# Kernel tuning notes

Hardware: AMD Instinct MI355X
Metric: run time of the kernel (lower is better)

The kernel has to match this reference:

```python
import jax, jax.numpy as jnp
import numpy as np

WINDOW = 8
NUM_HEADS = 12


def setup_inputs() -> dict:
    key = jax.random.key(0)
    k1, k2, k3 = jax.random.split(key, 3)
    B, H, W, C = 32, 64, 64, 384
    x = jax.random.normal(k1, (B, H, W, C), dtype=jnp.float32)
    w_qkv = jax.random.normal(k2, (C, 3 * C), dtype=jnp.float32) * (C ** -0.5)
    w_proj = jax.random.normal(k3, (C, C), dtype=jnp.float32) * (C ** -0.5)
    b_proj = jnp.zeros((C,), dtype=jnp.float32)
    return {"x": x, "w_qkv": w_qkv, "w_proj": w_proj, "b_proj": b_proj}


def window_partition(x, ws):
    B, H, W, C = x.shape
    x = x.reshape(B, H // ws, ws, W // ws, ws, C)
    x = x.transpose(0, 1, 3, 2, 4, 5)  # [B, nH, nW, ws, ws, C]
    return x.reshape(-1, ws * ws, C)


def window_reverse(x, ws, H, W):
    nWin = (H // ws) * (W // ws)
    B = x.shape[0] // nWin
    C = x.shape[2]
    x = x.reshape(B, H // ws, W // ws, ws, ws, C)
    x = x.transpose(0, 1, 3, 2, 4, 5)
    return x.reshape(B, H, W, C)


def reference(x, w_qkv, w_proj, b_proj):
    B, H, W, C = x.shape
    ws = WINDOW
    nh = NUM_HEADS
    hd = C // nh
    scale = hd ** -0.5
    N = ws * ws

    xw = window_partition(x, ws)                      # [nW*B, N, C]
    qkv = xw @ w_qkv                                  # [nW*B, N, 3C]
    qkv = qkv.reshape(-1, N, 3, nh, hd)
    qkv = qkv.transpose(2, 0, 3, 1, 4)                # [3, nW*B, nh, N, hd]
    q, k, v = qkv[0], qkv[1], qkv[2]

    attn = jnp.einsum('whnd,whmd->whnm', q, k) * scale  # [nW*B, nh, N, N]
    attn = jax.nn.softmax(attn, axis=-1)
    out = jnp.einsum('whnm,whmd->whnd', attn, v)         # [nW*B, nh, N, hd]
    out = out.transpose(0, 2, 1, 3).reshape(-1, N, C)    # [nW*B, N, C]
    out = out @ w_proj + b_proj
    return window_reverse(out, ws, H, W)
```

## Files before the change

kernel.cpp:

```cpp
#include <hip/hip_runtime.h>


typedef __attribute__((ext_vector_type(8))) short bf16x8;
typedef __attribute__((ext_vector_type(4))) float f32x4;
typedef __attribute__((ext_vector_type(4))) short short4_t;

__device__ __forceinline__ short f2bf(float f) {
    union { float f; unsigned u; } v; v.f = f;
    unsigned r = v.u + 0x7fffu + ((v.u >> 16) & 1u);
    return (short)(r >> 16);
}

__device__ __forceinline__ unsigned pk2(float a, float b) {
    return ((unsigned)(unsigned short)f2bf(b) << 16) | (unsigned short)f2bf(a);
}

__device__ __forceinline__ f32x4 mfma16(bf16x8 a, bf16x8 b, f32x4 c) {
    return __builtin_amdgcn_mfma_f32_16x16x32_bf16(a, b, c, 0, 0, 0);
}

__device__ __forceinline__ short4_t pack4(f32x4 v) {
    short4_t s;
    s.x = f2bf(v[0]); s.y = f2bf(v[1]); s.z = f2bf(v[2]); s.w = f2bf(v[3]);
    return s;
}

__device__ __forceinline__ void gload_lds16(const void* g, void* l) {
    __builtin_amdgcn_global_load_lds(
        (const __attribute__((address_space(1))) unsigned int*)g,
        (__attribute__((address_space(3))) unsigned int*)l, 16, 0, 0);
}

__global__ void prep_weights(const float* __restrict__ wqkv, const float* __restrict__ wproj,
                             short* __restrict__ wq_sw, short* __restrict__ wp_t) {
    const int QKV_ELEMS = 12 * 96 * 384;
    int i = blockIdx.x * 256 + threadIdx.x;
    if (i < QKV_ELEMS) {
        int h = i / (96 * 384);
        int o = i % (96 * 384);
        int row = o / 384;
        int kb = ((o % 384) * 2) ^ ((row & 7) << 4);
        int k = kb >> 1;
        int col = (row >> 5) * 384 + h * 32 + (row & 31);
        float w = wqkv[k * 1152 + col];
        if (row < 32) w *= 0.17677669529663687f;
        wq_sw[i] = f2bf(w);
    } else if (i < QKV_ELEMS + 384 * 384) {
        int j = i - QKV_ELEMS;
        int n = j / 384, k = j % 384;
        wp_t[j] = f2bf(wproj[k * 384 + n]);
    }
}

__global__ __launch_bounds__(1024)
void qkv_attn(const float* __restrict__ x, const short* __restrict__ wq_sw,
              short* __restrict__ y_sw) {
    __shared__ short Wl[96 * 384];
    __shared__ short k_s[4][64 * 40];
    __shared__ short v_t[4][32 * 72];
    __shared__ short ps[4][64 * 72];

    const int tid   = threadIdx.x;
    const int lane  = tid & 63;
    const int wv    = tid >> 6;
    const int col16 = lane & 15;
    const int kgrp  = lane >> 4;
    const int wwin  = wv >> 2;
    const int quad  = wv & 3;

    const int win = blockIdx.x * 4 + wwin;
    const int b = win >> 6, wi = win & 63, whr = wi >> 3, wwc = wi & 7;
    const float* xbase = x + (((b * 64) + whr * 8) * 64 + wwc * 8) * 384;

    for (int i = wv; i < 72; i += 16)
        gload_lds16(wq_sw + i * 512 + lane * 8, &Wl[i * 512]);

    bf16x8 xf[12];
    {
        int t = quad * 16 + col16;
        const float* xr = xbase + ((t >> 3) * 64 + (t & 7)) * 384;
#pragma unroll
        for (int kk = 0; kk < 12; ++kk) {
            const float* p0 = xr + kk * 32 + kgrp * 8;
            float4 a = *reinterpret_cast<const float4*>(p0);
            float4 c = *reinterpret_cast<const float4*>(p0 + 4);
            bf16x8 f;
            f[0] = f2bf(a.x); f[1] = f2bf(a.y); f[2] = f2bf(a.z); f[3] = f2bf(a.w);
            f[4] = f2bf(c.x); f[5] = f2bf(c.y); f[6] = f2bf(c.z); f[7] = f2bf(c.w);
            xf[kk] = f;
        }
    }

    const int g = win * 64 + quad * 16 + col16;
    const int mtile = g >> 7, yrow = g & 127;
    char* ybase = (char*)y_sw + (size_t)mtile * 98304 + (size_t)yrow * 128;

    for (int h = 0; h < 12; ++h) {
        __syncthreads();

        f32x4 acc[6];
#pragma unroll
        for (int i = 0; i < 6; ++i) acc[i] = (f32x4){0.f, 0.f, 0.f, 0.f};
#pragma unroll
        for (int kk = 0; kk < 12; ++kk) {
            const int kbyte = (kk * 32 + kgrp * 8) * 2;
#pragma unroll
            for (int rd = 0; rd < 6; ++rd) {
                const int row = (rd >> 1) * 32 + (rd & 1) * 16 + col16;
                const bf16x8 wf = *reinterpret_cast<const bf16x8*>(
                    (const char*)Wl + row * 768 + (kbyte ^ ((row & 7) << 4)));
                if (rd < 4) acc[rd] = mfma16(wf, xf[kk], acc[rd]);
                else        acc[rd] = mfma16(xf[kk], wf, acc[rd]);
            }
        }
        bf16x8 qa;
        {
            unsigned A0 = pk2(acc[0][0], acc[0][1]);
            unsigned A1 = pk2(acc[0][2], acc[0][3]);
            unsigned B0 = pk2(acc[1][0], acc[1][1]);
            unsigned B1 = pk2(acc[1][2], acc[1][3]);
            int s0 = ((kgrp & 1) * 2) * 16 + col16;
            int a0 = __shfl((int)A0, s0, 64),      a1 = __shfl((int)A1, s0, 64);
            int a2 = __shfl((int)A0, s0 + 16, 64), a3 = __shfl((int)A1, s0 + 16, 64);
            int b0 = __shfl((int)B0, s0, 64),      b1 = __shfl((int)B1, s0, 64);
            int b2 = __shfl((int)B0, s0 + 16, 64), b3 = __shfl((int)B1, s0 + 16, 64);
            union { int i[4]; bf16x8 v; } qu;
            const bool loHalf = (kgrp < 2);
            qu.i[0] = loHalf ? a0 : b0;
            qu.i[1] = loHalf ? a1 : b1;
            qu.i[2] = loHalf ? a2 : b2;
            qu.i[3] = loHalf ? a3 : b3;
            qa = qu.v;
        }
#pragma unroll
        for (int rd = 2; rd < 4; ++rd)
            *reinterpret_cast<short4_t*>(
                &k_s[wwin][(quad * 16 + col16) * 40 + (rd & 1) * 16 + kgrp * 4]) = pack4(acc[rd]);
#pragma unroll
        for (int d = 0; d < 2; ++d)
            *reinterpret_cast<short4_t*>(
                &v_t[wwin][(d * 16 + col16) * 72 + quad * 16 + kgrp * 4]) = pack4(acc[4 + d]);

        __syncthreads();

        if (h < 11) {
            const short* src = wq_sw + (h + 1) * (96 * 384);
            for (int i = wv; i < 72; i += 16)
                gload_lds16(src + i * 512 + lane * 8, &Wl[i * 512]);
        }

        f32x4 sc[4];
#pragma unroll
        for (int nt = 0; nt < 4; ++nt) {
            bf16x8 kf = *reinterpret_cast<const bf16x8*>(
                &k_s[wwin][(nt * 16 + col16) * 40 + kgrp * 8]);
            f32x4 z = (f32x4){0.f, 0.f, 0.f, 0.f};
            sc[nt] = mfma16(qa, kf, z);
        }
        float mx[4], sm[4];
#pragma unroll
        for (int r = 0; r < 4; ++r)
            mx[r] = fmaxf(fmaxf(sc[0][r], sc[1][r]), fmaxf(sc[2][r], sc[3][r]));
#pragma unroll
        for (int d = 1; d < 16; d <<= 1)
#pragma unroll
            for (int r = 0; r < 4; ++r) mx[r] = fmaxf(mx[r], __shfl_xor(mx[r], d, 16));
#pragma unroll
        for (int r = 0; r < 4; ++r) {
            sm[r] = 0.f;
#pragma unroll
            for (int nt = 0; nt < 4; ++nt) {
                sc[nt][r] = __expf(sc[nt][r] - mx[r]); sm[r] += sc[nt][r];
            }
        }
#pragma unroll
        for (int d = 1; d < 16; d <<= 1)
#pragma unroll
            for (int r = 0; r < 4; ++r) sm[r] += __shfl_xor(sm[r], d, 16);
#pragma unroll
        for (int r = 0; r < 4; ++r) {
            float inv = 1.0f / sm[r];
            int prow = quad * 16 + kgrp * 4 + r;
#pragma unroll
            for (int nt = 0; nt < 4; ++nt)
                ps[wwin][prow * 72 + nt * 16 + col16] = f2bf(sc[nt][r] * inv);
        }
        f32x4 o2[2];
        o2[0] = (f32x4){0.f, 0.f, 0.f, 0.f};
        o2[1] = (f32x4){0.f, 0.f, 0.f, 0.f};
#pragma unroll
        for (int kt = 0; kt < 2; ++kt) {
            bf16x8 pb = *reinterpret_cast<const bf16x8*>(
                &ps[wwin][(quad * 16 + col16) * 72 + kt * 32 + kgrp * 8]);
#pragma unroll
            for (int d = 0; d < 2; ++d) {
                bf16x8 va = *reinterpret_cast<const bf16x8*>(
                    &v_t[wwin][(d * 16 + col16) * 72 + kt * 32 + kgrp * 8]);
                o2[d] = mfma16(va, pb, o2[d]);
            }
        }
#pragma unroll
        for (int d = 0; d < 2; ++d) {
            int c0 = h * 32 + d * 16 + kgrp * 4;
            int kchunk = c0 >> 6;
            int koff = (2 * (c0 & 63)) ^ ((yrow & 7) << 4);
            *reinterpret_cast<short4_t*>(ybase + kchunk * 16384 + koff) = pack4(o2[d]);
        }
    }
}

__global__ __launch_bounds__(256)
void proj_gemm(const short* __restrict__ y_sw, const short* __restrict__ wp_t,
               const float* __restrict__ b_proj, float* __restrict__ out) {
    __shared__ short At[2][128 * 64];

    const int tid = threadIdx.x, lane = tid & 63, wv = tid >> 6;
    const int col16 = lane & 15, kgrp = lane >> 4;
    const int wm = wv >> 1, wn = wv & 1;
    const int mtile = blockIdx.x;
    const int nblk  = blockIdx.y;

    const short* asrc = y_sw + (size_t)mtile * 6 * 128 * 64;

    for (int i = wv; i < 16; i += 4)
        gload_lds16(asrc + i * 512 + lane * 8, &At[0][i * 512]);

    const short* bptr[4];
#pragma unroll
    for (int nt = 0; nt < 4; ++nt)
        bptr[nt] = wp_t + (size_t)(nblk * 128 + wn * 64 + nt * 16 + col16) * 384;

    f32x4 acc[4][4];
#pragma unroll
    for (int i = 0; i < 4; ++i)
#pragma unroll
        for (int j = 0; j < 4; ++j) acc[i][j] = (f32x4){0.f, 0.f, 0.f, 0.f};

    int cur = 0;
    for (int ks = 0; ks < 6; ++ks) {
        __syncthreads();
        if (ks < 5) {
            const short* src = asrc + (ks + 1) * (128 * 64);
            for (int i = wv; i < 16; i += 4)
                gload_lds16(src + i * 512 + lane * 8, &At[cur ^ 1][i * 512]);
        }
#pragma unroll
        for (int kk = 0; kk < 2; ++kk) {
            const int kbyte = kk * 64 + kgrp * 16;
            bf16x8 af[4];
#pragma unroll
            for (int mt = 0; mt < 4; ++mt) {
                const int r = wm * 64 + mt * 16 + col16;
                af[mt] = *reinterpret_cast<const bf16x8*>(
                    (const char*)At[cur] + r * 128 + (kbyte ^ ((r & 7) << 4)));
            }
#pragma unroll
            for (int nt = 0; nt < 4; ++nt) {
                bf16x8 bf = *reinterpret_cast<const bf16x8*>(bptr[nt] + ks * 64 + kk * 32 + kgrp * 8);
#pragma unroll
                for (int mt = 0; mt < 4; ++mt)
                    acc[mt][nt] = mfma16(af[mt], bf, acc[mt][nt]);
            }
        }
        cur ^= 1;
    }

#pragma unroll
    for (int nt = 0; nt < 4; ++nt) {
        int c = nblk * 128 + wn * 64 + nt * 16 + col16;
        float bias = b_proj[c];
#pragma unroll
        for (int mt = 0; mt < 4; ++mt) {
#pragma unroll
            for (int r = 0; r < 4; ++r) {
                int gg = mtile * 128 + wm * 64 + mt * 16 + kgrp * 4 + r;
                int win = gg >> 6, t = gg & 63;
                int b = win >> 6, whr = (win >> 3) & 7, wwc = win & 7;
                int orow = (b * 64 + whr * 8 + (t >> 3)) * 64 + wwc * 8 + (t & 7);
                out[(size_t)orow * 384 + c] = acc[mt][nt][r] + bias;
            }
        }
    }
}

__global__ __launch_bounds__(512, 2)
void win_attn_fused(const float* __restrict__ x, const short* __restrict__ wq_sw,
                    const short* __restrict__ wp_t, const float* __restrict__ b_proj,
                    float* __restrict__ out) {
    __shared__ short Wl[96 * 384];
    __shared__ short q_s[2][64 * 40];
    __shared__ short k_s[2][64 * 40];
    __shared__ short v_t[2][32 * 72];
    __shared__ short ps[2][64 * 72];

    const int tid   = threadIdx.x;
    const int lane  = tid & 63;
    const int wv    = tid >> 6;
    const int col16 = lane & 15;
    const int kgrp  = lane >> 4;
    const int wwin  = wv >> 2;
    const int q4    = wv & 3;
    const int wm    = q4 >> 1, wn = q4 & 1;

    const int win = blockIdx.x * 2 + wwin;
    const int b = win >> 6, wi = win & 63, whr = wi >> 3, wwc = wi & 7;
    const float* xbase = x + (((b * 64) + whr * 8) * 64 + wwc * 8) * 384;

    for (int i = 0; i < 9; ++i) {
        int chunk = wv * 9 + i;
        gload_lds16(wq_sw + chunk * 512 + lane * 8, &Wl[chunk * 512]);
    }
    bf16x8 xf[12];
    {
        int t = q4 * 16 + col16;
        const float* xr = xbase + ((t >> 3) * 64 + (t & 7)) * 384;
#pragma unroll
        for (int kk = 0; kk < 12; ++kk) {
            const float* p0 = xr + kk * 32 + kgrp * 8;
            float4 a = *reinterpret_cast<const float4*>(p0);
            float4 c = *reinterpret_cast<const float4*>(p0 + 4);
            bf16x8 f;
            f[0] = f2bf(a.x); f[1] = f2bf(a.y); f[2] = f2bf(a.z); f[3] = f2bf(a.w);
            f[4] = f2bf(c.x); f[5] = f2bf(c.y); f[6] = f2bf(c.z); f[7] = f2bf(c.w);
            xf[kk] = f;
        }
    }
    f32x4 pacc[2][12];
#pragma unroll
    for (int i = 0; i < 2; ++i)
#pragma unroll
        for (int j = 0; j < 12; ++j) pacc[i][j] = (f32x4){0.f, 0.f, 0.f, 0.f};

    for (int h = 0; h < 12; ++h) {
        __syncthreads();
        f32x4 acc[6];
#pragma unroll
        for (int i = 0; i < 6; ++i) acc[i] = (f32x4){0.f, 0.f, 0.f, 0.f};
#pragma unroll
        for (int kk = 0; kk < 12; ++kk) {
            const int kbyte = (kk * 32 + kgrp * 8) * 2;
#pragma unroll
            for (int rd = 0; rd < 6; ++rd) {
                const int row = (rd >> 1) * 32 + (rd & 1) * 16 + col16;
                const bf16x8 wf = *reinterpret_cast<const bf16x8*>(
                    (const char*)Wl + row * 768 + (kbyte ^ ((row & 7) << 4)));
                if (rd < 4) acc[rd] = mfma16(wf, xf[kk], acc[rd]);
                else        acc[rd] = mfma16(xf[kk], wf, acc[rd]);
            }
        }
#pragma unroll
        for (int rd = 0; rd < 4; ++rd) {
            short* dst = (rd < 2) ? q_s[wwin] : k_s[wwin];
            *reinterpret_cast<short4_t*>(
                &dst[(q4 * 16 + col16) * 40 + (rd & 1) * 16 + kgrp * 4]) = pack4(acc[rd]);
        }
#pragma unroll
        for (int d = 0; d < 2; ++d)
            *reinterpret_cast<short4_t*>(
                &v_t[wwin][(d * 16 + col16) * 72 + q4 * 16 + kgrp * 4]) = pack4(acc[4 + d]);

        __syncthreads();
        if (h < 11) {
            const short* src = wq_sw + (h + 1) * (96 * 384);
            for (int i = 0; i < 9; ++i) {
                int chunk = wv * 9 + i;
                gload_lds16(src + chunk * 512 + lane * 8, &Wl[chunk * 512]);
            }
        }
        bf16x8 qa = *reinterpret_cast<const bf16x8*>(
            &q_s[wwin][(q4 * 16 + col16) * 40 + kgrp * 8]);
        f32x4 sc[4];
#pragma unroll
        for (int nt = 0; nt < 4; ++nt) {
            bf16x8 kf = *reinterpret_cast<const bf16x8*>(
                &k_s[wwin][(nt * 16 + col16) * 40 + kgrp * 8]);
            f32x4 z = (f32x4){0.f, 0.f, 0.f, 0.f};
            sc[nt] = mfma16(qa, kf, z);
        }
        float mx[4], sm[4], p[4][4];
#pragma unroll
        for (int r = 0; r < 4; ++r)
            mx[r] = fmaxf(fmaxf(sc[0][r], sc[1][r]), fmaxf(sc[2][r], sc[3][r]));
#pragma unroll
        for (int d = 1; d < 16; d <<= 1)
#pragma unroll
            for (int r = 0; r < 4; ++r) mx[r] = fmaxf(mx[r], __shfl_xor(mx[r], d, 16));
#pragma unroll
        for (int r = 0; r < 4; ++r) {
            sm[r] = 0.f;
#pragma unroll
            for (int nt = 0; nt < 4; ++nt) { p[nt][r] = __expf(sc[nt][r] - mx[r]); sm[r] += p[nt][r]; }
        }
#pragma unroll
        for (int d = 1; d < 16; d <<= 1)
#pragma unroll
            for (int r = 0; r < 4; ++r) sm[r] += __shfl_xor(sm[r], d, 16);
#pragma unroll
        for (int r = 0; r < 4; ++r) {
            float inv = 1.0f / sm[r];
            int prow = q4 * 16 + kgrp * 4 + r;
#pragma unroll
            for (int nt = 0; nt < 4; ++nt)
                ps[wwin][prow * 72 + nt * 16 + col16] = f2bf(p[nt][r] * inv);
        }
        f32x4 o2[2];
        o2[0] = (f32x4){0.f, 0.f, 0.f, 0.f};
        o2[1] = (f32x4){0.f, 0.f, 0.f, 0.f};
#pragma unroll
        for (int kt = 0; kt < 2; ++kt) {
            bf16x8 pb = *reinterpret_cast<const bf16x8*>(
                &ps[wwin][(q4 * 16 + col16) * 72 + kt * 32 + kgrp * 8]);
#pragma unroll
            for (int d = 0; d < 2; ++d) {
                bf16x8 va = *reinterpret_cast<const bf16x8*>(
                    &v_t[wwin][(d * 16 + col16) * 72 + kt * 32 + kgrp * 8]);
                o2[d] = mfma16(va, pb, o2[d]);
            }
        }
#pragma unroll
        for (int d = 0; d < 2; ++d)
            *reinterpret_cast<short4_t*>(
                &ps[wwin][(q4 * 16 + col16) * 72 + d * 16 + kgrp * 4]) = pack4(o2[d]);
        __syncthreads();
#pragma unroll
        for (int mt = 0; mt < 2; ++mt) {
            bf16x8 ya = *reinterpret_cast<const bf16x8*>(
                &ps[wwin][(wm * 32 + mt * 16 + col16) * 72 + kgrp * 8]);
#pragma unroll
            for (int nt = 0; nt < 12; ++nt) {
                bf16x8 wb = *reinterpret_cast<const bf16x8*>(
                    &wp_t[(wn * 192 + nt * 16 + col16) * 384 + h * 32 + kgrp * 8]);
                pacc[mt][nt] = mfma16(ya, wb, pacc[mt][nt]);
            }
        }
    }
#pragma unroll
    for (int nt = 0; nt < 12; ++nt) {
        int c = wn * 192 + nt * 16 + col16;
        float bias = b_proj[c];
#pragma unroll
        for (int mt = 0; mt < 2; ++mt) {
#pragma unroll
            for (int r = 0; r < 4; ++r) {
                int token = wm * 32 + mt * 16 + kgrp * 4 + r;
                int hh = whr * 8 + (token >> 3);
                int ww2 = wwc * 8 + (token & 7);
                out[(((b * 64) + hh) * 64 + ww2) * 384 + c] = pacc[mt][nt][r] + bias;
            }
        }
    }
}

extern "C" void kernel_launch(void* const* d_in, const int* in_sizes, int n_in,
                              void* d_out, int out_size, void* d_ws, size_t ws_size,
                              hipStream_t stream) {
    const float* x     = (const float*)d_in[0];
    const float* wqkv  = (const float*)d_in[1];
    const float* wproj = (const float*)d_in[2];
    const float* bproj = (const float*)d_in[3];

    short* wq_sw = (short*)d_ws;
    short* wp_t  = wq_sw + 12 * 96 * 384;
    short* y_sw  = wp_t + 384 * 384;
    const size_t need = (size_t)(12 * 96 * 384 + 384 * 384) * 2 + (size_t)1024 * 6 * 128 * 128;

    prep_weights<<<2304, 256, 0, stream>>>(wqkv, wproj, wq_sw, wp_t);
    if (ws_size >= need) {
        qkv_attn<<<512, 1024, 0, stream>>>(x, wq_sw, y_sw);
        proj_gemm<<<dim3(1024, 3), 256, 0, stream>>>(y_sw, wp_t, bproj, (float*)d_out);
    } else {
        win_attn_fused<<<1024, 512, 0, stream>>>(x, wq_sw, wp_t, bproj, (float*)d_out);
    }
}
```

Before: 390.7 us.

## Split QKV projection across warps by output rows to reuse weight fragments

Reassigns warps in the fused QKV-attention kernel so each warp handles 32 tokens and a subset of the Q/K/V output rows, rather than 16 tokens and all 96 rows. Each weight fragment loaded from LDS now feeds two MFMAs, which halves LDS weight reads per MFMA. Softmax is handled by the Q/K warps while the V warps prefetch the next head's weights. The cost is twice the x registers per thread, one more block-wide barrier per head, and an uneven split of work between warp groups during the softmax phase.

```diff
diff --git a/kernel.cpp b/kernel.cpp
--- a/kernel.cpp
+++ b/kernel.cpp
@@ -62,140 +62,214 @@
 
     const int tid   = threadIdx.x;
     const int lane  = tid & 63;
-    const int wv    = tid >> 6;
+    const int wid   = tid >> 6;
     const int col16 = lane & 15;
     const int kgrp  = lane >> 4;
-    const int wwin  = wv >> 2;
-    const int quad  = wv & 3;
-
-    const int win = blockIdx.x * 4 + wwin;
-    const int b = win >> 6, wi = win & 63, whr = wi >> 3, wwc = wi & 7;
-    const float* xbase = x + (((b * 64) + whr * 8) * 64 + wwc * 8) * 384;
-
-    for (int i = wv; i < 72; i += 16)
+    const int m     = wid >> 3;
+    const int n     = wid & 7;
+    const int w     = n >> 1;
+    const int th    = n & 1;
+
+    const int w2    = wid >> 2;
+    const int quad  = wid & 3;
+
+    for (int i = wid; i < 72; i += 16)
         gload_lds16(wq_sw + i * 512 + lane * 8, &Wl[i * 512]);
 
-    bf16x8 xf[12];
+    bf16x8 xf[2][12];
     {
-        int t = quad * 16 + col16;
-        const float* xr = xbase + ((t >> 3) * 64 + (t & 7)) * 384;
-#pragma unroll
-        for (int kk = 0; kk < 12; ++kk) {
-            const float* p0 = xr + kk * 32 + kgrp * 8;
-            float4 a = *reinterpret_cast<const float4*>(p0);
-            float4 c = *reinterpret_cast<const float4*>(p0 + 4);
-            bf16x8 f;
-            f[0] = f2bf(a.x); f[1] = f2bf(a.y); f[2] = f2bf(a.z); f[3] = f2bf(a.w);
-            f[4] = f2bf(c.x); f[5] = f2bf(c.y); f[6] = f2bf(c.z); f[7] = f2bf(c.w);
-            xf[kk] = f;
-        }
-    }
-
-    const int g = win * 64 + quad * 16 + col16;
-    const int mtile = g >> 7, yrow = g & 127;
+        const int winA = blockIdx.x * 4 + w;
+        const int bA = winA >> 6, wiA = winA & 63, whrA = wiA >> 3, wwcA = wiA & 7;
+        const float* xbase = x + (((bA * 64) + whrA * 8) * 64 + wwcA * 8) * 384;
+#pragma unroll
+        for (int nt = 0; nt < 2; ++nt) {
+            int t = th * 32 + nt * 16 + col16;
+            const float* xr = xbase + ((t >> 3) * 64 + (t & 7)) * 384;
+#pragma unroll
+            for (int kk = 0; kk < 12; ++kk) {
+                const float* p0 = xr + kk * 32 + kgrp * 8;
+                float4 a = *reinterpret_cast<const float4*>(p0);
+                float4 c = *reinterpret_cast<const float4*>(p0 + 4);
+                bf16x8 f;
+                f[0] = f2bf(a.x); f[1] = f2bf(a.y); f[2] = f2bf(a.z); f[3] = f2bf(a.w);
+                f[4] = f2bf(c.x); f[5] = f2bf(c.y); f[6] = f2bf(c.z); f[7] = f2bf(c.w);
+                xf[nt][kk] = f;
+            }
+        }
+    }
+
+    const int winB = blockIdx.x * 4 + w2;
+    const int gtok = winB * 64 + quad * 16 + col16;
+    const int mtile = gtok >> 7, yrow = gtok & 127;
     char* ybase = (char*)y_sw + (size_t)mtile * 98304 + (size_t)yrow * 128;
 
+    const int tokbase = th * 32;
+
     for (int h = 0; h < 12; ++h) {
         __syncthreads();
 
-        f32x4 acc[6];
-#pragma unroll
-        for (int i = 0; i < 6; ++i) acc[i] = (f32x4){0.f, 0.f, 0.f, 0.f};
-#pragma unroll
-        for (int kk = 0; kk < 12; ++kk) {
-            const int kbyte = (kk * 32 + kgrp * 8) * 2;
-#pragma unroll
-            for (int rd = 0; rd < 6; ++rd) {
-                const int row = (rd >> 1) * 32 + (rd & 1) * 16 + col16;
-                const bf16x8 wf = *reinterpret_cast<const bf16x8*>(
-                    (const char*)Wl + row * 768 + (kbyte ^ ((row & 7) << 4)));
-                if (rd < 4) acc[rd] = mfma16(wf, xf[kk], acc[rd]);
-                else        acc[rd] = mfma16(xf[kk], wf, acc[rd]);
-            }
-        }
-        bf16x8 qa;
-        {
-            unsigned A0 = pk2(acc[0][0], acc[0][1]);
-            unsigned A1 = pk2(acc[0][2], acc[0][3]);
-            unsigned B0 = pk2(acc[1][0], acc[1][1]);
-            unsigned B1 = pk2(acc[1][2], acc[1][3]);
-            int s0 = ((kgrp & 1) * 2) * 16 + col16;
-            int a0 = __shfl((int)A0, s0, 64),      a1 = __shfl((int)A1, s0, 64);
-            int a2 = __shfl((int)A0, s0 + 16, 64), a3 = __shfl((int)A1, s0 + 16, 64);
-            int b0 = __shfl((int)B0, s0, 64),      b1 = __shfl((int)B1, s0, 64);
-            int b2 = __shfl((int)B0, s0 + 16, 64), b3 = __shfl((int)B1, s0 + 16, 64);
-            union { int i[4]; bf16x8 v; } qu;
-            const bool loHalf = (kgrp < 2);
-            qu.i[0] = loHalf ? a0 : b0;
-            qu.i[1] = loHalf ? a1 : b1;
-            qu.i[2] = loHalf ? a2 : b2;
-            qu.i[3] = loHalf ? a3 : b3;
-            qa = qu.v;
-        }
-#pragma unroll
-        for (int rd = 2; rd < 4; ++rd)
-            *reinterpret_cast<short4_t*>(
-                &k_s[wwin][(quad * 16 + col16) * 40 + (rd & 1) * 16 + kgrp * 4]) = pack4(acc[rd]);
-#pragma unroll
-        for (int d = 0; d < 2; ++d)
-            *reinterpret_cast<short4_t*>(
-                &v_t[wwin][(d * 16 + col16) * 72 + quad * 16 + kgrp * 4]) = pack4(acc[4 + d]);
-
-        __syncthreads();
-
-        if (h < 11) {
-            const short* src = wq_sw + (h + 1) * (96 * 384);
-            for (int i = wv; i < 72; i += 16)
-                gload_lds16(src + i * 512 + lane * 8, &Wl[i * 512]);
-        }
-
-        f32x4 sc[4];
-#pragma unroll
-        for (int nt = 0; nt < 4; ++nt) {
-            bf16x8 kf = *reinterpret_cast<const bf16x8*>(
-                &k_s[wwin][(nt * 16 + col16) * 40 + kgrp * 8]);
-            f32x4 z = (f32x4){0.f, 0.f, 0.f, 0.f};
-            sc[nt] = mfma16(qa, kf, z);
-        }
-        float mx[4], sm[4];
-#pragma unroll
-        for (int r = 0; r < 4; ++r)
-            mx[r] = fmaxf(fmaxf(sc[0][r], sc[1][r]), fmaxf(sc[2][r], sc[3][r]));
-#pragma unroll
-        for (int d = 1; d < 16; d <<= 1)
-#pragma unroll
-            for (int r = 0; r < 4; ++r) mx[r] = fmaxf(mx[r], __shfl_xor(mx[r], d, 16));
-#pragma unroll
-        for (int r = 0; r < 4; ++r) {
-            sm[r] = 0.f;
-#pragma unroll
-            for (int nt = 0; nt < 4; ++nt) {
-                sc[nt][r] = __expf(sc[nt][r] - mx[r]); sm[r] += sc[nt][r];
-            }
-        }
-#pragma unroll
-        for (int d = 1; d < 16; d <<= 1)
-#pragma unroll
-            for (int r = 0; r < 4; ++r) sm[r] += __shfl_xor(sm[r], d, 16);
-#pragma unroll
-        for (int r = 0; r < 4; ++r) {
-            float inv = 1.0f / sm[r];
-            int prow = quad * 16 + kgrp * 4 + r;
-#pragma unroll
-            for (int nt = 0; nt < 4; ++nt)
-                ps[wwin][prow * 72 + nt * 16 + col16] = f2bf(sc[nt][r] * inv);
-        }
+        f32x4 acc[3][2];
+#pragma unroll
+        for (int i = 0; i < 3; ++i)
+#pragma unroll
+            for (int j = 0; j < 2; ++j) acc[i][j] = (f32x4){0.f, 0.f, 0.f, 0.f};
+
+        if (m == 0) {
+#pragma unroll
+            for (int kk = 0; kk < 12; ++kk) {
+                const int kbyte = kk * 64 + kgrp * 16;
+#pragma unroll
+                for (int mt = 0; mt < 3; ++mt) {
+                    const int row = mt * 16 + col16;
+                    const bf16x8 wf = *reinterpret_cast<const bf16x8*>(
+                        (const char*)Wl + row * 768 + (kbyte ^ ((row & 7) << 4)));
+#pragma unroll
+                    for (int nt = 0; nt < 2; ++nt)
+                        acc[mt][nt] = mfma16(wf, xf[nt][kk], acc[mt][nt]);
+                }
+            }
+        } else {
+#pragma unroll
+            for (int kk = 0; kk < 12; ++kk) {
+                const int kbyte = kk * 64 + kgrp * 16;
+                {
+                    const int row = 48 + col16;
+                    const bf16x8 wf = *reinterpret_cast<const bf16x8*>(
+                        (const char*)Wl + row * 768 + (kbyte ^ ((row & 7) << 4)));
+#pragma unroll
+                    for (int nt = 0; nt < 2; ++nt)
+                        acc[0][nt] = mfma16(wf, xf[nt][kk], acc[0][nt]);
+                }
+#pragma unroll
+                for (int vt = 0; vt < 2; ++vt) {
+                    const int row = 64 + vt * 16 + col16;
+                    const bf16x8 wf = *reinterpret_cast<const bf16x8*>(
+                        (const char*)Wl + row * 768 + (kbyte ^ ((row & 7) << 4)));
+#pragma unroll
+                    for (int nt = 0; nt < 2; ++nt)
+                        acc[1 + vt][nt] = mfma16(xf[nt][kk], wf, acc[1 + vt][nt]);
+                }
+            }
+        }
+
+        bf16x8 qa[2];
+        if (m == 0) {
+#pragma unroll
+            for (int nt = 0; nt < 2; ++nt) {
+                unsigned A0 = pk2(acc[0][nt][0], acc[0][nt][1]);
+                unsigned A1 = pk2(acc[0][nt][2], acc[0][nt][3]);
+                unsigned B0 = pk2(acc[1][nt][0], acc[1][nt][1]);
+                unsigned B1 = pk2(acc[1][nt][2], acc[1][nt][3]);
+                int s0 = ((kgrp & 1) * 2) * 16 + col16;
+                int a0 = __shfl((int)A0, s0, 64),      a1 = __shfl((int)A1, s0, 64);
+                int a2 = __shfl((int)A0, s0 + 16, 64), a3 = __shfl((int)A1, s0 + 16, 64);
+                int b0 = __shfl((int)B0, s0, 64),      b1 = __shfl((int)B1, s0, 64);
+                int b2 = __shfl((int)B0, s0 + 16, 64), b3 = __shfl((int)B1, s0 + 16, 64);
+                union { int i[4]; bf16x8 v; } qu;
+                const bool loHalf = (kgrp < 2);
+                qu.i[0] = loHalf ? a0 : b0;
+                qu.i[1] = loHalf ? a1 : b1;
+                qu.i[2] = loHalf ? a2 : b2;
+                qu.i[3] = loHalf ? a3 : b3;
+                qa[nt] = qu.v;
+            }
+#pragma unroll
+            for (int nt = 0; nt < 2; ++nt)
+                *reinterpret_cast<short4_t*>(
+                    &k_s[w][(tokbase + nt * 16 + col16) * 40 + kgrp * 4]) = pack4(acc[2][nt]);
+        } else {
+#pragma unroll
+            for (int nt = 0; nt < 2; ++nt)
+                *reinterpret_cast<short4_t*>(
+                    &k_s[w][(tokbase + nt * 16 + col16) * 40 + 16 + kgrp * 4]) = pack4(acc[0][nt]);
+#pragma unroll
+            for (int vt = 0; vt < 2; ++vt)
+#pragma unroll
+                for (int nt = 0; nt < 2; ++nt)
+                    *reinterpret_cast<short4_t*>(
+                        &v_t[w][(vt * 16 + col16) * 72 + tokbase + nt * 16 + kgrp * 4]) =
+                        pack4(acc[1 + vt][nt]);
+        }
+
+        __syncthreads();
+
+        if (m == 1) {
+            if (h < 11) {
+                const short* src = wq_sw + (h + 1) * (96 * 384);
+                for (int i = n; i < 72; i += 8)
+                    gload_lds16(src + i * 512 + lane * 8, &Wl[i * 512]);
+            }
+        } else {
+            bf16x8 kf[4];
+#pragma unroll
+            for (int kt = 0; kt < 4; ++kt)
+                kf[kt] = *reinterpret_cast<const bf16x8*>(
+                    &k_s[w][(kt * 16 + col16) * 40 + kgrp * 8]);
+            f32x4 sc[2][4];
+#pragma unroll
+            for (int nt = 0; nt < 2; ++nt)
+#pragma unroll
+                for (int kt = 0; kt < 4; ++kt) {
+                    f32x4 z = (f32x4){0.f, 0.f, 0.f, 0.f};
+                    sc[nt][kt] = mfma16(qa[nt], kf[kt], z);
+                }
+            float mx[2][4], sm[2][4];
+#pragma unroll
+            for (int nt = 0; nt < 2; ++nt)
+#pragma unroll
+                for (int r = 0; r < 4; ++r)
+                    mx[nt][r] = fmaxf(fmaxf(sc[nt][0][r], sc[nt][1][r]),
+                                      fmaxf(sc[nt][2][r], sc[nt][3][r]));
+#pragma unroll
+            for (int d = 1; d < 16; d <<= 1)
+#pragma unroll
+                for (int nt = 0; nt < 2; ++nt)
+#pragma unroll
+                    for (int r = 0; r < 4; ++r)
+                        mx[nt][r] = fmaxf(mx[nt][r], __shfl_xor(mx[nt][r], d, 16));
+#pragma unroll
+            for (int nt = 0; nt < 2; ++nt)
+#pragma unroll
+                for (int r = 0; r < 4; ++r) {
+                    sm[nt][r] = 0.f;
+#pragma unroll
+                    for (int kt = 0; kt < 4; ++kt) {
+                        sc[nt][kt][r] = __expf(sc[nt][kt][r] - mx[nt][r]);
+                        sm[nt][r] += sc[nt][kt][r];
+                    }
+                }
+#pragma unroll
+            for (int d = 1; d < 16; d <<= 1)
+#pragma unroll
+                for (int nt = 0; nt < 2; ++nt)
+#pragma unroll
+                    for (int r = 0; r < 4; ++r)
+                        sm[nt][r] += __shfl_xor(sm[nt][r], d, 16);
+#pragma unroll
+            for (int nt = 0; nt < 2; ++nt)
+#pragma unroll
+                for (int r = 0; r < 4; ++r) {
+                    float inv = 1.0f / sm[nt][r];
+                    int prow = tokbase + nt * 16 + kgrp * 4 + r;
+#pragma unroll
+                    for (int kt = 0; kt < 4; ++kt)
+                        ps[w][prow * 72 + kt * 16 + col16] = f2bf(sc[nt][kt][r] * inv);
+                }
+        }
+
+        __syncthreads();
+
         f32x4 o2[2];
         o2[0] = (f32x4){0.f, 0.f, 0.f, 0.f};
         o2[1] = (f32x4){0.f, 0.f, 0.f, 0.f};
 #pragma unroll
         for (int kt = 0; kt < 2; ++kt) {
             bf16x8 pb = *reinterpret_cast<const bf16x8*>(
-                &ps[wwin][(quad * 16 + col16) * 72 + kt * 32 + kgrp * 8]);
+                &ps[w2][(quad * 16 + col16) * 72 + kt * 32 + kgrp * 8]);
 #pragma unroll
             for (int d = 0; d < 2; ++d) {
                 bf16x8 va = *reinterpret_cast<const bf16x8*>(
-                    &v_t[wwin][(d * 16 + col16) * 72 + kt * 32 + kgrp * 8]);
+                    &v_t[w2][(d * 16 + col16) * 72 + kt * 32 + kgrp * 8]);
                 o2[d] = mfma16(va, pb, o2[d]);
             }
         }
```

New measurement: 604.0 us. 54.6% more time.
